# Performance work log

Measured on AMD Instinct MI355X. Metric: run time of the kernel, lower is better.

## Reference

```python
import jax, jax.numpy as jnp
import numpy as np

B, N, H, E, WF = 2048, 30, 256, 256, 32
TANH_C = 10.0  # tanh_exploration


def _mask_modify(m):
    # if a row is all True, un-mask the last column
    all_true = jnp.all(m, axis=1)
    return m.at[:, -1].set(m[:, -1] & ~all_true)


def _lstm_cell(x, h, c, W_ih, W_hh, b_ih, b_hh):
    gates = x @ W_ih.T + b_ih + h @ W_hh.T + b_hh
    i, f, g, o = jnp.split(gates, 4, axis=1)  # torch LSTMCell gate order
    c_new = jax.nn.sigmoid(f) * c + jax.nn.sigmoid(i) * jnp.tanh(g)
    h_new = jax.nn.sigmoid(o) * jnp.tanh(c_new)
    return h_new, c_new


def _attention(query, ref, Wq, bq, Wr, br, v, C=None):
    # query [B,H], ref [B,H,N] (context permuted)
    q = query @ Wq.T + bq                                        # [B,H]
    e = jnp.einsum('oh,bhn->bon', Wr, ref) + br[None, :, None]   # 1x1 conv
    u = jnp.einsum('h,bhn->bn', v, jnp.tanh(q[:, :, None] + e))  # [B,N]
    logits = C * jnp.tanh(u) if C is not None else u
    return e, logits


def setup_inputs() -> dict:
    key = jax.random.key(0)
    ks = jax.random.split(key, 24)
    s = 0.06  # ~1/sqrt(H) init scale
    n = lambda k, sh: jax.random.normal(k, sh, dtype=jnp.float32)
    return {
        'decoder_input': n(ks[0], (B, E)),
        'embedded_inputs': n(ks[1], (N, B, E)),
        'h0': n(ks[2], (B, H)),
        'c0': n(ks[3], (B, H)),
        'context': n(ks[4], (N, B, H)),
        'embed_cou': n(ks[5], (B, WF)),
        'D': jax.random.uniform(ks[6], (B, N, N), dtype=jnp.float32),
        'W_ih': n(ks[7], (4 * H, E)) * s,
        'W_hh': n(ks[8], (4 * H, H)) * s,
        'b_ih': n(ks[9], (4 * H,)) * s,
        'b_hh': n(ks[10], (4 * H,)) * s,
        'W_merge': n(ks[11], (H, H + WF)) * s,
        'b_merge': n(ks[12], (H,)) * s,
        'Wq_p': n(ks[13], (H, H)) * s,
        'bq_p': n(ks[14], (H,)) * s,
        'Wr_p': n(ks[15], (H, H)) * s,
        'br_p': n(ks[16], (H,)) * s,
        'v_p': n(ks[17], (H,)) * s,
        'Wq_g': n(ks[18], (H, H)) * s,
        'bq_g': n(ks[19], (H,)) * s,
        'Wr_g': n(ks[20], (H, H)) * s,
        'br_g': n(ks[21], (H,)) * s,
        'v_g': n(ks[22], (H,)) * s,
        'V_reach_mask_t': jnp.zeros((B, N), dtype=bool),
        'start_idx': jax.random.randint(ks[23], (B,), 0, N),
        'k_min_nodes': 3,
    }


def reference(decoder_input, embedded_inputs, h0, c0, context, embed_cou, D,
              W_ih, W_hh, b_ih, b_hh, W_merge, b_merge,
              Wq_p, bq_p, Wr_p, br_p, v_p,
              Wq_g, bq_g, Wr_g, br_g, v_g,
              V_reach_mask_t, start_idx, k_min_nodes):
    ref = jnp.transpose(context, (1, 2, 0))  # [B,H,N]
    arangeB = jnp.arange(B)
    arangeN = jnp.arange(N)

    def step(carry, _):
        h, c, mask, idxs, dec_in, knn_row = carry
        # --- update_knn_mask ('n-1'): builds the row used at the NEXT step ---
        Eb = D[arangeB, idxs]                                  # [B,N]
        weighted = Eb * (~mask).astype(Eb.dtype)
        valid = jnp.sum(~mask, axis=1) > k_min_nodes
        far = jnp.argmax(weighted, axis=1)
        next_row = (arangeN[None, :] == far[:, None]) & valid[:, None]
        # --- recurrence: update_mask + check_mask ---
        lm = mask.at[arangeB, idxs].set(True)
        lm = _mask_modify(_mask_modify(lm))
        full_mask = lm | knn_row
        # LSTM step + worker-feature merge
        hy, cy = _lstm_cell(dec_in, h, c, W_ih, W_hh, b_ih, b_hh)
        g_l = jnp.concatenate([hy, embed_cou], axis=1) @ W_merge.T + b_merge
        # one glimpse (n_glimpses=1)
        e_g, lg = _attention(g_l, ref, Wq_g, bq_g, Wr_g, br_g, v_g)
        lg = jnp.where(full_mask, -jnp.inf, lg)
        g_l = jnp.einsum('bhn,bn->bh', e_g, jax.nn.softmax(lg, axis=1))
        # pointer (use_tanh with C)
        _, lp = _attention(g_l, ref, Wq_p, bq_p, Wr_p, br_p, v_p, C=TANH_C)
        lp = jnp.where(full_mask, -jnp.inf, lp)
        log_p = jax.nn.log_softmax(lp, axis=1)
        new_idxs = jnp.argmax(log_p, axis=1)  # greedy decode
        new_dec = embedded_inputs[new_idxs, arangeB]  # [B,E]
        return (hy, cy, lm, new_idxs, new_dec, next_row), (log_p, new_idxs)

    init = (h0, c0, V_reach_mask_t, start_idx, decoder_input,
            jnp.zeros_like(V_reach_mask_t))
    (_, _, mask, _, _, _), (logps, sels) = jax.lax.scan(step, init, None, length=N)
    return jnp.swapaxes(logps, 0, 1), jnp.swapaxes(sels, 0, 1), mask
```

## Files before the change

kernel.cpp:

```cpp
#include <hip/hip_runtime.h>
#include <hip/hip_bf16.h>
#include <math.h>

#define B 2048
#define NN 30
#define H 256
#define EDIM 256
#define G4 1024

typedef __attribute__((ext_vector_type(8))) short short8;
typedef __attribute__((ext_vector_type(4))) float f32x4;

__device__ __forceinline__ float fsig(float x) {
    return __fdividef(1.f, 1.f + __expf(-x));
}
__device__ __forceinline__ float ftanh(float x) {
    return 1.f - __fdividef(2.f, __expf(2.f * x) + 1.f);
}

__global__ __launch_bounds__(256)
void gemm_big(const float* __restrict__ A,
              const float* __restrict__ W0, const float* __restrict__ W1,
              const float* __restrict__ W2,
              const float* __restrict__ b0, const float* __restrict__ b1,
              const float* __restrict__ b2,
              float* __restrict__ C0, float* __restrict__ C1,
              float* __restrict__ C2)
{
    __shared__ __align__(16) float As[16][128];
    __shared__ __align__(16) float Ws[16][128];
    int tid = threadIdx.x;
    int tx = tid & 15, ty = (tid >> 4) & 15;

    int lin = blockIdx.y * 6 + blockIdx.x;
    int v = (lin & 7) * 360 + (lin >> 3);
    int m0 = (v / 6) << 7;
    int nblk = v % 6;
    int part = nblk >> 1;
    int nin = (nblk & 1) << 7;
    const float* W    = part == 0 ? W0 : part == 1 ? W1 : W2;
    const float* bias = part == 0 ? b0 : part == 1 ? b1 : b2;
    float* C          = part == 0 ? C0 : part == 1 ? C1 : C2;

    int lr = tid >> 1;
    int lk8 = (tid & 1) << 3;
    const float* arow = A + (long)(m0 + lr) * 256 + lk8;
    const float* wrow = W + (long)(nin + lr) * 256 + lk8;
    float4 a0 = *(const float4*)(arow);
    float4 a1 = *(const float4*)(arow + 4);
    float4 w0 = *(const float4*)(wrow);
    float4 w1 = *(const float4*)(wrow + 4);
    float acc[8][8] = {};

    for (int k0 = 0; k0 < 256; k0 += 16) {
        As[lk8 + 0][lr] = a0.x; As[lk8 + 1][lr] = a0.y;
        As[lk8 + 2][lr] = a0.z; As[lk8 + 3][lr] = a0.w;
        As[lk8 + 4][lr] = a1.x; As[lk8 + 5][lr] = a1.y;
        As[lk8 + 6][lr] = a1.z; As[lk8 + 7][lr] = a1.w;
        Ws[lk8 + 0][lr] = w0.x; Ws[lk8 + 1][lr] = w0.y;
        Ws[lk8 + 2][lr] = w0.z; Ws[lk8 + 3][lr] = w0.w;
        Ws[lk8 + 4][lr] = w1.x; Ws[lk8 + 5][lr] = w1.y;
        Ws[lk8 + 6][lr] = w1.z; Ws[lk8 + 7][lr] = w1.w;
        __syncthreads();
        if (k0 + 16 < 256) {
            a0 = *(const float4*)(arow + k0 + 16);
            a1 = *(const float4*)(arow + k0 + 20);
            w0 = *(const float4*)(wrow + k0 + 16);
            w1 = *(const float4*)(wrow + k0 + 20);
        }
        #pragma unroll
        for (int k = 0; k < 16; ++k) {
            float4 af0 = *(const float4*)&As[k][ty << 2];
            float4 af1 = *(const float4*)&As[k][64 + (ty << 2)];
            float4 wf0 = *(const float4*)&Ws[k][tx << 2];
            float4 wf1 = *(const float4*)&Ws[k][64 + (tx << 2)];
            float av[8] = {af0.x, af0.y, af0.z, af0.w, af1.x, af1.y, af1.z, af1.w};
            float wv[8] = {wf0.x, wf0.y, wf0.z, wf0.w, wf1.x, wf1.y, wf1.z, wf1.w};
            #pragma unroll
            for (int i = 0; i < 8; ++i)
                #pragma unroll
                for (int j = 0; j < 8; ++j)
                    acc[i][j] = fmaf(av[i], wv[j], acc[i][j]);
        }
        __syncthreads();
    }

    float bj[8];
    #pragma unroll
    for (int j = 0; j < 8; ++j) {
        int cj = nin + ((j < 4) ? (tx << 2) + j : 64 + (tx << 2) + j - 4);
        bj[j] = bias[cj];
    }
    #pragma unroll
    for (int i = 0; i < 8; ++i) {
        int m = m0 + ((i < 4) ? (ty << 2) + i : 64 + (ty << 2) + i - 4);
        float* crow = C + (long)m * 256 + nin;
        float4 v0 = make_float4(acc[i][0] + bj[0], acc[i][1] + bj[1],
                                acc[i][2] + bj[2], acc[i][3] + bj[3]);
        float4 v1 = make_float4(acc[i][4] + bj[4], acc[i][5] + bj[5],
                                acc[i][6] + bj[6], acc[i][7] + bj[7]);
        *(float4*)&crow[(tx << 2)] = v0;
        *(float4*)&crow[64 + (tx << 2)] = v1;
    }
}

__global__ __launch_bounds__(256)
void gates_mfma(const unsigned short* __restrict__ dhi, const unsigned short* __restrict__ dlo,
                const unsigned short* __restrict__ hhi, const unsigned short* __restrict__ hlo,
                const unsigned short* __restrict__ Whi, const unsigned short* __restrict__ Wlo,
                const float* __restrict__ bsum, const float* __restrict__ cin,
                float* __restrict__ hout, float* __restrict__ cout,
                unsigned short* __restrict__ hohi, unsigned short* __restrict__ holo)
{
    __shared__ __align__(16) unsigned short Ah[128][40];
    __shared__ __align__(16) unsigned short Al[128][40];
    __shared__ __align__(16) unsigned short Bh[64][40];
    __shared__ __align__(16) unsigned short Bl[64][40];

    int tid = threadIdx.x;
    int w = tid >> 6, l = tid & 63;
    int lin = blockIdx.x;
    int v = (lin & 7) * 32 + (lin >> 3);
    int m0 = (v >> 4) << 7;
    int u0 = (v & 15) << 4;

    int arow = tid >> 1;
    int akb  = (tid & 1) << 4;
    int brw  = tid >> 2;
    int bkb  = (tid & 3) << 3;
    int wrow = ((brw >> 4) << 8) + u0 + (brw & 15);
    const unsigned short* wph = Whi + (long)wrow * 512 + bkb;
    const unsigned short* wpl = Wlo + (long)wrow * 512 + bkb;

    int fk = (l >> 4) << 3;
    int fr = l & 15;

    f32x4 acc[2][4];
    #pragma unroll
    for (int i = 0; i < 2; ++i)
        #pragma unroll
        for (int j = 0; j < 4; ++j)
            acc[i][j] = (f32x4){0.f, 0.f, 0.f, 0.f};

    for (int kt = 0; kt < 16; ++kt) {
        int k0 = kt << 5;
        const unsigned short* sah; const unsigned short* sal; int kk;
        if (k0 < 256) { sah = dhi; sal = dlo; kk = k0; }
        else          { sah = hhi; sal = hlo; kk = k0 - 256; }
        long abase = (long)(m0 + arow) * 256 + kk + akb;
        short8 a0 = *(const short8*)&sah[abase];
        short8 a1 = *(const short8*)&sah[abase + 8];
        short8 a2 = *(const short8*)&sal[abase];
        short8 a3 = *(const short8*)&sal[abase + 8];
        short8 b0 = *(const short8*)&wph[k0];
        short8 b1 = *(const short8*)&wpl[k0];
        __syncthreads();
        *(short8*)&Ah[arow][akb]     = a0;
        *(short8*)&Ah[arow][akb + 8] = a1;
        *(short8*)&Al[arow][akb]     = a2;
        *(short8*)&Al[arow][akb + 8] = a3;
        *(short8*)&Bh[brw][bkb] = b0;
        *(short8*)&Bl[brw][bkb] = b1;
        __syncthreads();

        short8 aH[2], aL[2], bH[4], bL[4];
        #pragma unroll
        for (int ms = 0; ms < 2; ++ms) {
            int r = (w << 5) + (ms << 4) + fr;
            aH[ms] = *(const short8*)&Ah[r][fk];
            aL[ms] = *(const short8*)&Al[r][fk];
        }
        #pragma unroll
        for (int s = 0; s < 4; ++s) {
            int r = (s << 4) + fr;
            bH[s] = *(const short8*)&Bh[r][fk];
            bL[s] = *(const short8*)&Bl[r][fk];
        }
        #pragma unroll
        for (int ms = 0; ms < 2; ++ms)
            #pragma unroll
            for (int s = 0; s < 4; ++s)
                acc[ms][s] = __builtin_amdgcn_mfma_f32_16x16x32_bf16(aH[ms], bH[s], acc[ms][s], 0, 0, 0);
        #pragma unroll
        for (int ms = 0; ms < 2; ++ms)
            #pragma unroll
            for (int s = 0; s < 4; ++s)
                acc[ms][s] = __builtin_amdgcn_mfma_f32_16x16x32_bf16(aH[ms], bL[s], acc[ms][s], 0, 0, 0);
        #pragma unroll
        for (int ms = 0; ms < 2; ++ms)
            #pragma unroll
            for (int s = 0; s < 4; ++s)
                acc[ms][s] = __builtin_amdgcn_mfma_f32_16x16x32_bf16(aL[ms], bH[s], acc[ms][s], 0, 0, 0);
    }

    int u = u0 + fr;
    float bI = bsum[u], bF = bsum[256 + u], bG = bsum[512 + u], bO = bsum[768 + u];
    #pragma unroll
    for (int ms = 0; ms < 2; ++ms) {
        #pragma unroll
        for (int r = 0; r < 4; ++r) {
            int m = m0 + (w << 5) + (ms << 4) + ((l >> 4) << 2) + r;
            float gi = acc[ms][0][r] + bI;
            float gf = acc[ms][1][r] + bF;
            float gg = acc[ms][2][r] + bG;
            float go = acc[ms][3][r] + bO;
            float cv = cin[(long)m * H + u];
            float cn = fsig(gf) * cv + fsig(gi) * ftanh(gg);
            float hn = fsig(go) * ftanh(cn);
            cout[(long)m * H + u] = cn;
            hout[(long)m * H + u] = hn;
            unsigned hb = __float_as_uint(hn);
            hohi[(long)m * H + u] = (unsigned short)(hb >> 16);
            float lo = hn - __uint_as_float(hb & 0xffff0000u);
            holo[(long)m * H + u] = (unsigned short)(__float_as_uint(lo) >> 16);
        }
    }
}

__global__ __launch_bounds__(256)
void gemm_qg(const float* __restrict__ A, const float* __restrict__ W,
             const float* __restrict__ addend, float* __restrict__ C)
{
    __shared__ __align__(16) float As[2][16][36];
    __shared__ __align__(16) float Ws[2][16][68];
    int tid = threadIdx.x;
    int tx = tid & 15, ty = tid >> 4;

    int lin = blockIdx.y * 4 + blockIdx.x;
    int v = (lin & 7) * 32 + (lin >> 3);
    int m0 = (v >> 2) << 5;
    int n0 = (v & 3) << 6;

    int lrA = tid >> 3, lkA = (tid & 7) << 1;
    int lrW = tid >> 2, lkW = (tid & 3) << 2;
    const float* arow = A + (long)(m0 + lrA) * 256;
    const float* wrow = W + (long)(n0 + lrW) * 256;

    float2 av = *(const float2*)(arow + lkA);
    float4 wv = *(const float4*)(wrow + lkW);
    As[0][lkA + 0][lrA] = av.x; As[0][lkA + 1][lrA] = av.y;
    Ws[0][lkW + 0][lrW] = wv.x; Ws[0][lkW + 1][lrW] = wv.y;
    Ws[0][lkW + 2][lrW] = wv.z; Ws[0][lkW + 3][lrW] = wv.w;
    __syncthreads();

    float acc[2][4] = {};
    int p = 0;
    for (int k0 = 0; k0 < 256; k0 += 16) {
        float2 nav; float4 nwv;
        bool more = (k0 + 16) < 256;
        if (more) {
            nav = *(const float2*)(arow + k0 + 16 + lkA);
            nwv = *(const float4*)(wrow + k0 + 16 + lkW);
        }
        #pragma unroll
        for (int k = 0; k < 16; ++k) {
            float2 a2 = *(const float2*)&As[p][k][ty << 1];
            float4 b4 = *(const float4*)&Ws[p][k][tx << 2];
            acc[0][0] = fmaf(a2.x, b4.x, acc[0][0]);
            acc[0][1] = fmaf(a2.x, b4.y, acc[0][1]);
            acc[0][2] = fmaf(a2.x, b4.z, acc[0][2]);
            acc[0][3] = fmaf(a2.x, b4.w, acc[0][3]);
            acc[1][0] = fmaf(a2.y, b4.x, acc[1][0]);
            acc[1][1] = fmaf(a2.y, b4.y, acc[1][1]);
            acc[1][2] = fmaf(a2.y, b4.z, acc[1][2]);
            acc[1][3] = fmaf(a2.y, b4.w, acc[1][3]);
        }
        if (more) {
            int q = p ^ 1;
            As[q][lkA + 0][lrA] = nav.x; As[q][lkA + 1][lrA] = nav.y;
            Ws[q][lkW + 0][lrW] = nwv.x; Ws[q][lkW + 1][lrW] = nwv.y;
            Ws[q][lkW + 2][lrW] = nwv.z; Ws[q][lkW + 3][lrW] = nwv.w;
        }
        __syncthreads();
        p ^= 1;
    }

    #pragma unroll
    for (int i = 0; i < 2; ++i) {
        int m = m0 + (ty << 1) + i;
        const float* ad = &addend[(long)m * 256 + n0 + (tx << 2)];
        float4 adv = *(const float4*)ad;
        float4 o = make_float4(acc[i][0] + adv.x, acc[i][1] + adv.y,
                               acc[i][2] + adv.z, acc[i][3] + adv.w);
        *(float4*)&C[(long)m * 256 + n0 + (tx << 2)] = o;
    }
}

__global__ void init_state(const unsigned char* __restrict__ vr, const int* __restrict__ start,
                           unsigned char* __restrict__ mask, unsigned char* __restrict__ knn,
                           int* __restrict__ idxs)
{
    int t = blockIdx.x * 256 + threadIdx.x;
    if (t < B * NN) { mask[t] = vr[t] ? 1 : 0; knn[t] = 0; }
    if (t < B) idxs[t] = start[t];
}

__global__ void prep_wsplit(const float* __restrict__ Wih, const float* __restrict__ Whh,
                            const float* __restrict__ bih, const float* __restrict__ bhh,
                            unsigned short* __restrict__ Whi, unsigned short* __restrict__ Wlo,
                            float* __restrict__ bsum)
{
    int n = blockIdx.x, k = threadIdx.x;
    float a = Wih[(long)n * H + k];
    unsigned ab = __float_as_uint(a);
    Whi[(long)n * 512 + k] = (unsigned short)(ab >> 16);
    float alo = a - __uint_as_float(ab & 0xffff0000u);
    Wlo[(long)n * 512 + k] = (unsigned short)(__float_as_uint(alo) >> 16);
    float b = Whh[(long)n * H + k];
    unsigned bb = __float_as_uint(b);
    Whi[(long)n * 512 + 256 + k] = (unsigned short)(bb >> 16);
    float blo = b - __uint_as_float(bb & 0xffff0000u);
    Wlo[(long)n * 512 + 256 + k] = (unsigned short)(__float_as_uint(blo) >> 16);
    if (k == 0) bsum[n] = bih[n] + bhh[n];
}

__global__ void conv_pair(const float* __restrict__ x,
                          unsigned short* __restrict__ xhi, unsigned short* __restrict__ xlo)
{
    int t = blockIdx.x * 256 + threadIdx.x;
    float a = x[t];
    unsigned ab = __float_as_uint(a);
    xhi[t] = (unsigned short)(ab >> 16);
    float lo = a - __uint_as_float(ab & 0xffff0000u);
    xlo[t] = (unsigned short)(__float_as_uint(lo) >> 16);
}

__global__ void prep_compose1(const float* __restrict__ Wqg, const float* __restrict__ Wm,
                              float* __restrict__ W1c)
{
    int h = blockIdx.x, k = threadIdx.x;
    float a = 0.f;
    for (int j = 0; j < H; ++j) a = fmaf(Wqg[(long)h * H + j], Wm[(long)j * 288 + k], a);
    W1c[(long)h * H + k] = a;
}

__global__ void prep_compose2(const float* __restrict__ Wqg, const float* __restrict__ Wm,
                              const float* __restrict__ bm, const float* __restrict__ bqg,
                              float* __restrict__ W2c, float* __restrict__ bc)
{
    int h = blockIdx.x, w = threadIdx.x;
    if (w < 32) {
        float a = 0.f;
        for (int j = 0; j < H; ++j) a = fmaf(Wqg[(long)h * H + j], Wm[(long)j * 288 + 256 + w], a);
        W2c[h * 32 + w] = a;
    } else if (w == 32) {
        float a = 0.f;
        for (int j = 0; j < H; ++j) a = fmaf(Wqg[(long)h * H + j], bm[j], a);
        bc[h] = a + bqg[h];
    }
}

__global__ __launch_bounds__(256)
void prep_qc(const float* __restrict__ cou, const float* __restrict__ W2c,
             const float* __restrict__ bc, float* __restrict__ qc)
{
    __shared__ float sWT[32 * 256];
    __shared__ float sb[256];
    int b = blockIdx.x, h = threadIdx.x;
    for (int i = h; i < 32 * 256; i += 256) {
        int hh = i >> 5, ww = i & 31;
        sWT[ww * 256 + hh] = W2c[i];
    }
    sb[h] = bc[h];
    __syncthreads();
    const float* cr = cou + (long)b * 32;
    float a = sb[h];
    for (int w = 0; w < 32; ++w) a = fmaf(cr[w], sWT[w * 256 + h], a);
    qc[(long)b * H + h] = a;
}

__global__ void prep_composeF(const float* __restrict__ Wqp, const float* __restrict__ Wrg,
                              const float* __restrict__ brg, float* __restrict__ WFc,
                              float* __restrict__ bFc)
{
    int f = blockIdx.x, k = threadIdx.x;
    float a = 0.f;
    for (int j = 0; j < H; ++j) a = fmaf(Wqp[(long)f * H + j], Wrg[(long)j * H + k], a);
    WFc[(long)f * H + k] = a;
    if (k == 0) {
        float s = 0.f;
        for (int j = 0; j < H; ++j) s = fmaf(Wqp[(long)f * H + j], brg[j], s);
        bFc[f] = s;
    }
}

__global__ __launch_bounds__(512)
void mega_attn2(const float* __restrict__ eg, const float* __restrict__ ep,
                const float* __restrict__ F, const float* __restrict__ qg,
                const float* __restrict__ vg, const float* __restrict__ vp,
                const float* __restrict__ bqp,
                const float* __restrict__ D, const int* __restrict__ kminp,
                unsigned char* __restrict__ mask, unsigned char* __restrict__ knn,
                const float* __restrict__ emb,
                float* __restrict__ out, int step,
                int* __restrict__ idxs,
                unsigned short* __restrict__ dechi, unsigned short* __restrict__ declo)
{
    int b = blockIdx.x, tid = threadIdx.x;
    int wv = tid >> 6, lane = tid & 63;
    __shared__ float sU[32], sP[32];
    __shared__ float sQp[H];
    __shared__ float sPar[2][H];
    __shared__ unsigned char sFull[32];
    __shared__ int sSel;

    float4 q4  = ((const float4*)(qg + (long)b * H))[lane];
    float4 vg4 = ((const float4*)vg)[lane];
    float4 vp4 = ((const float4*)vp)[lane];

    if (tid < 64) {
        bool in = lane < NN;
        int idx = idxs[b];
        int kmin = *kminp;
        unsigned char m = in ? mask[b * NN + lane] : (unsigned char)1;
        float dv = in ? D[((long)b * NN + idx) * NN + lane] : 0.f;
        unsigned long long unm = __ballot(in && !m);
        int cnt = __popcll(unm);
        bool valid = cnt > kmin;
        float bw = (in && !m) ? dv : (in ? 0.f : -1.f);
        int bi = in ? lane : 1000;
        #pragma unroll
        for (int off = 32; off; off >>= 1) {
            float ow = __shfl_down(bw, off, 64);
            int oi = __shfl_down(bi, off, 64);
            if (ow > bw || (ow == bw && oi < bi)) { bw = ow; bi = oi; }
        }
        int far = __shfl(bi, 0, 64);
        unsigned char mnew = (in && lane == idx) ? 1 : m;
        #pragma unroll
        for (int rep = 0; rep < 2; ++rep) {
            bool allm = (__ballot(in && !mnew) == 0ull);
            if (allm && lane == NN - 1) mnew = 0;
        }
        unsigned char kn = in ? knn[b * NN + lane] : 0;
        if (in) {
            sFull[lane] = (mnew | kn) ? 1 : 0;
            mask[b * NN + lane] = mnew;
            knn[b * NN + lane] = (lane == far && valid) ? 1 : 0;
        }
    }
    __syncthreads();

    for (int n = wv; n < NN; n += 8) {
        if (sFull[n]) continue;
        float4 e4 = ((const float4*)(eg + ((long)n * B + b) * H))[lane];
        float s = vg4.x * ftanh(q4.x + e4.x);
        s = fmaf(vg4.y, ftanh(q4.y + e4.y), s);
        s = fmaf(vg4.z, ftanh(q4.z + e4.z), s);
        s = fmaf(vg4.w, ftanh(q4.w + e4.w), s);
        #pragma unroll
        for (int off = 32; off; off >>= 1) s += __shfl_down(s, off, 64);
        if (lane == 0) sU[n] = s;
    }
    __syncthreads();

    if (tid < 64) {
        bool in = tid < NN;
        bool f = in ? (sFull[tid] != 0) : true;
        float u = (in && !f) ? sU[tid] : -INFINITY;
        float mx = u;
        #pragma unroll
        for (int off = 32; off; off >>= 1) mx = fmaxf(mx, __shfl_down(mx, off, 64));
        mx = __shfl(mx, 0, 64);
        float p = (in && !f) ? __expf(u - mx) : 0.f;
        float sum = p;
        #pragma unroll
        for (int off = 32; off; off >>= 1) sum += __shfl_down(sum, off, 64);
        sum = __shfl(sum, 0, 64);
        if (in) sP[tid] = p / sum;
    }
    __syncthreads();

    {
        int half = tid >> 8, hh = tid & 255;
        float a = 0.f;
        #pragma unroll
        for (int n = 0; n < 15; ++n) {
            int nn = half * 15 + n;
            float pn = sP[nn];
            if (pn != 0.f)
                a = fmaf(pn, F[((long)nn * B + b) * H + hh], a);
        }
        sPar[half][hh] = a;
    }
    __syncthreads();
    if (tid < 256) sQp[tid] = bqp[tid] + sPar[0][tid] + sPar[1][tid];
    __syncthreads();

    float4 qp4 = ((const float4*)sQp)[lane];
    for (int n = wv; n < NN; n += 8) {
        if (sFull[n]) continue;
        float4 e4 = ((const float4*)(ep + ((long)n * B + b) * H))[lane];
        float s = vp4.x * ftanh(qp4.x + e4.x);
        s = fmaf(vp4.y, ftanh(qp4.y + e4.y), s);
        s = fmaf(vp4.z, ftanh(qp4.z + e4.z), s);
        s = fmaf(vp4.w, ftanh(qp4.w + e4.w), s);
        #pragma unroll
        for (int off = 32; off; off >>= 1) s += __shfl_down(s, off, 64);
        if (lane == 0) sU[n] = 10.f * ftanh(s);
    }
    __syncthreads();

    if (tid < 64) {
        bool in = tid < NN;
        bool f = in ? (sFull[tid] != 0) : true;
        float l = (in && !f) ? sU[tid] : -INFINITY;
        float mx = l; int bi = in ? tid : 1000;
        #pragma unroll
        for (int off = 32; off; off >>= 1) {
            float om = __shfl_down(mx, off, 64);
            int oi = __shfl_down(bi, off, 64);
            if (om > mx || (om == mx && oi < bi)) { mx = om; bi = oi; }
        }
        mx = __shfl(mx, 0, 64);
        bi = __shfl(bi, 0, 64);
        float pe = (in && !f) ? __expf(l - mx) : 0.f;
        float sum = pe;
        #pragma unroll
        for (int off = 32; off; off >>= 1) sum += __shfl_down(sum, off, 64);
        sum = __shfl(sum, 0, 64);
        float lse = mx + __logf(sum);
        if (tid == 0) {
            idxs[b] = bi;
            out[(long)B * NN * NN + (long)b * NN + step] = (float)bi;
            sSel = bi;
        }
        if (in)
            out[(long)b * NN * NN + (long)step * NN + tid] =
                f ? -1e30f : (l - lse);
    }
    __syncthreads();

    if (tid < 256) {
        int sel = sSel;
        float d = emb[((long)sel * B + b) * EDIM + tid];
        unsigned db = __float_as_uint(d);
        dechi[(long)b * H + tid] = (unsigned short)(db >> 16);
        float lo = d - __uint_as_float(db & 0xffff0000u);
        declo[(long)b * H + tid] = (unsigned short)(__float_as_uint(lo) >> 16);
    }
}

__global__ void mask_out(const unsigned char* __restrict__ mask, float* __restrict__ out)
{
    int t = blockIdx.x * 256 + threadIdx.x;
    if (t < B * NN)
        out[(long)B * NN * NN + (long)B * NN + t] = mask[t] ? 1.f : 0.f;
}

extern "C" void kernel_launch(void* const* d_in, const int* in_sizes, int n_in,
                              void* d_out, int out_size, void* d_ws, size_t ws_size,
                              hipStream_t stream)
{
    const float* decoder_input = (const float*)d_in[0];
    const float* embedded     = (const float*)d_in[1];
    const float* h0           = (const float*)d_in[2];
    const float* c0           = (const float*)d_in[3];
    const float* context      = (const float*)d_in[4];
    const float* embed_cou    = (const float*)d_in[5];
    const float* D            = (const float*)d_in[6];
    const float* W_ih         = (const float*)d_in[7];
    const float* W_hh         = (const float*)d_in[8];
    const float* b_ih         = (const float*)d_in[9];
    const float* b_hh         = (const float*)d_in[10];
    const float* W_merge      = (const float*)d_in[11];
    const float* b_merge      = (const float*)d_in[12];
    const float* Wq_p         = (const float*)d_in[13];
    const float* bq_p         = (const float*)d_in[14];
    const float* Wr_p         = (const float*)d_in[15];
    const float* br_p         = (const float*)d_in[16];
    const float* v_p          = (const float*)d_in[17];
    const float* Wq_g         = (const float*)d_in[18];
    const float* bq_g         = (const float*)d_in[19];
    const float* Wr_g         = (const float*)d_in[20];
    const float* br_g         = (const float*)d_in[21];
    const float* v_g          = (const float*)d_in[22];
    const unsigned char* vreach = (const unsigned char*)d_in[23];
    const int* start_idx      = (const int*)d_in[24];
    const int* kminp          = (const int*)d_in[25];

    float* ws = (float*)d_ws;
    size_t o = 0;
    float* eg     = ws + o; o += (size_t)B * NN * H;
    float* ep     = ws + o; o += (size_t)B * NN * H;
    float* Fbuf   = ws + o; o += (size_t)B * NN * H;
    float* hb0    = ws + o; o += (size_t)B * H;
    float* hb1    = ws + o; o += (size_t)B * H;
    float* cb0    = ws + o; o += (size_t)B * H;
    float* cb1    = ws + o; o += (size_t)B * H;
    float* qbuf   = ws + o; o += (size_t)B * H;
    float* qc     = ws + o; o += (size_t)B * H;
    float* W1c    = ws + o; o += (size_t)H * H;
    float* W2c    = ws + o; o += (size_t)H * 32;
    float* bc     = ws + o; o += (size_t)H;
    float* WFc    = ws + o; o += (size_t)H * H;
    float* bFc    = ws + o; o += (size_t)H;
    float* bsum   = ws + o; o += (size_t)G4;
    unsigned short* Whi  = (unsigned short*)(ws + o); o += (size_t)G4 * 512 / 2;
    unsigned short* Wlo  = (unsigned short*)(ws + o); o += (size_t)G4 * 512 / 2;
    unsigned short* dechi = (unsigned short*)(ws + o); o += (size_t)B * H / 2;
    unsigned short* declo = (unsigned short*)(ws + o); o += (size_t)B * H / 2;
    unsigned short* hAhi = (unsigned short*)(ws + o); o += (size_t)B * H / 2;
    unsigned short* hAlo = (unsigned short*)(ws + o); o += (size_t)B * H / 2;
    unsigned short* hBhi = (unsigned short*)(ws + o); o += (size_t)B * H / 2;
    unsigned short* hBlo = (unsigned short*)(ws + o); o += (size_t)B * H / 2;
    unsigned char* maskb = (unsigned char*)(ws + o);
    unsigned char* knnb  = maskb + (size_t)B * NN;
    int* idxs = (int*)(knnb + (size_t)B * NN + 64);

    float* out = (float*)d_out;

    init_state<<<dim3((B * NN + 255) / 256), dim3(256), 0, stream>>>(
        vreach, start_idx, maskb, knnb, idxs);

    prep_wsplit<<<dim3(G4), dim3(256), 0, stream>>>(W_ih, W_hh, b_ih, b_hh,
                                                    Whi, Wlo, bsum);
    conv_pair<<<dim3(B * H / 256), dim3(256), 0, stream>>>(decoder_input, dechi, declo);
    conv_pair<<<dim3(B * H / 256), dim3(256), 0, stream>>>(h0, hAhi, hAlo);
    prep_compose1<<<dim3(H), dim3(256), 0, stream>>>(Wq_g, W_merge, W1c);
    prep_compose2<<<dim3(H), dim3(64), 0, stream>>>(Wq_g, W_merge, b_merge, bq_g,
                                                    W2c, bc);
    prep_qc<<<dim3(B), dim3(256), 0, stream>>>(embed_cou, W2c, bc, qc);
    prep_composeF<<<dim3(H), dim3(256), 0, stream>>>(Wq_p, Wr_g, br_g, WFc, bFc);

    gemm_big<<<dim3(6, (B * NN) / 128), dim3(256), 0, stream>>>(
        context, Wr_g, Wr_p, WFc, br_g, br_p, bFc, eg, ep, Fbuf);

    const float* cin = c0;
    unsigned short* hInHi = hAhi; unsigned short* hInLo = hAlo;
    unsigned short* hOutHi = hBhi; unsigned short* hOutLo = hBlo;

    for (int step = 0; step < NN; ++step) {
        int p = step & 1;
        float* hout = p ? hb1 : hb0;
        float* cout = p ? cb1 : cb0;

        gates_mfma<<<dim3(256), dim3(256), 0, stream>>>(
            dechi, declo, hInHi, hInLo, Whi, Wlo, bsum, cin,
            hout, cout, hOutHi, hOutLo);

        gemm_qg<<<dim3(4, B / 32), dim3(256), 0, stream>>>(
            hout, W1c, qc, qbuf);

        mega_attn2<<<dim3(B), dim3(512), 0, stream>>>(
            eg, ep, Fbuf, qbuf, v_g, v_p, bq_p, D, kminp,
            maskb, knnb, embedded, out, step, idxs, dechi, declo);

        cin = cout;
        unsigned short* th = hInHi; hInHi = hOutHi; hOutHi = th;
        unsigned short* tl = hInLo; hInLo = hOutLo; hOutLo = tl;
    }

    mask_out<<<dim3((B * NN + 255) / 256), dim3(256), 0, stream>>>(maskb, out);
}
```

Before: 2.518 ms.

## Rewrite big FP32 GEMM with split-bf16 MFMA (3-way split, 6 products)

```diff
diff --git a/kernel.cpp b/kernel.cpp
--- a/kernel.cpp
+++ b/kernel.cpp
@@ -16,6 +16,18 @@
 }
 __device__ __forceinline__ float ftanh(float x) {
     return 1.f - __fdividef(2.f, __expf(2.f * x) + 1.f);
+}
+
+__device__ __forceinline__ void split3(float a, unsigned short& h,
+                                       unsigned short& m_, unsigned short& l_)
+{
+    unsigned ab = __float_as_uint(a);
+    h = (unsigned short)(ab >> 16);
+    float r1 = a - __uint_as_float(ab & 0xffff0000u);
+    unsigned rb = __float_as_uint(r1);
+    m_ = (unsigned short)(rb >> 16);
+    float r2 = r1 - __uint_as_float(rb & 0xffff0000u);
+    l_ = (unsigned short)(__float_as_uint(r2) >> 16);
 }
 
 __global__ __launch_bounds__(256)
@@ -27,10 +39,15 @@
               float* __restrict__ C0, float* __restrict__ C1,
               float* __restrict__ C2)
 {
-    __shared__ __align__(16) float As[16][128];
-    __shared__ __align__(16) float Ws[16][128];
+    __shared__ __align__(16) unsigned short Ah[128][40];
+    __shared__ __align__(16) unsigned short Am[128][40];
+    __shared__ __align__(16) unsigned short Al[128][40];
+    __shared__ __align__(16) unsigned short Bh[128][40];
+    __shared__ __align__(16) unsigned short Bm[128][40];
+    __shared__ __align__(16) unsigned short Bl[128][40];
+
     int tid = threadIdx.x;
-    int tx = tid & 15, ty = (tid >> 4) & 15;
+    int w = tid >> 6, l = tid & 63;
 
     int lin = blockIdx.y * 6 + blockIdx.x;
     int v = (lin & 7) * 360 + (lin >> 3);
@@ -42,65 +59,111 @@
     const float* bias = part == 0 ? b0 : part == 1 ? b1 : b2;
     float* C          = part == 0 ? C0 : part == 1 ? C1 : C2;
 
-    int lr = tid >> 1;
-    int lk8 = (tid & 1) << 3;
-    const float* arow = A + (long)(m0 + lr) * 256 + lk8;
-    const float* wrow = W + (long)(nin + lr) * 256 + lk8;
-    float4 a0 = *(const float4*)(arow);
-    float4 a1 = *(const float4*)(arow + 4);
-    float4 w0 = *(const float4*)(wrow);
-    float4 w1 = *(const float4*)(wrow + 4);
-    float acc[8][8] = {};
-
-    for (int k0 = 0; k0 < 256; k0 += 16) {
-        As[lk8 + 0][lr] = a0.x; As[lk8 + 1][lr] = a0.y;
-        As[lk8 + 2][lr] = a0.z; As[lk8 + 3][lr] = a0.w;
-        As[lk8 + 4][lr] = a1.x; As[lk8 + 5][lr] = a1.y;
-        As[lk8 + 6][lr] = a1.z; As[lk8 + 7][lr] = a1.w;
-        Ws[lk8 + 0][lr] = w0.x; Ws[lk8 + 1][lr] = w0.y;
-        Ws[lk8 + 2][lr] = w0.z; Ws[lk8 + 3][lr] = w0.w;
-        Ws[lk8 + 4][lr] = w1.x; Ws[lk8 + 5][lr] = w1.y;
-        Ws[lk8 + 6][lr] = w1.z; Ws[lk8 + 7][lr] = w1.w;
+    int srow = tid >> 1;
+    int skb  = (tid & 1) << 4;
+    const float* arow = A + (long)(m0 + srow) * 256 + skb;
+    const float* wrow = W + (long)(nin + srow) * 256 + skb;
+
+    int fr = l & 15;
+    int fk = (l >> 4) << 3;
+
+    f32x4 acc[2][8];
+    #pragma unroll
+    for (int i = 0; i < 2; ++i)
+        #pragma unroll
+        for (int j = 0; j < 8; ++j)
+            acc[i][j] = (f32x4){0.f, 0.f, 0.f, 0.f};
+
+    for (int kt = 0; kt < 8; ++kt) {
+        int k0 = kt << 5;
+        float4 a4[4], w4[4];
+        #pragma unroll
+        for (int i = 0; i < 4; ++i) {
+            a4[i] = *(const float4*)(arow + k0 + (i << 2));
+            w4[i] = *(const float4*)(wrow + k0 + (i << 2));
+        }
         __syncthreads();
-        if (k0 + 16 < 256) {
-            a0 = *(const float4*)(arow + k0 + 16);
-            a1 = *(const float4*)(arow + k0 + 20);
-            w0 = *(const float4*)(wrow + k0 + 16);
-            w1 = *(const float4*)(wrow + k0 + 20);
-        }
-        #pragma unroll
-        for (int k = 0; k < 16; ++k) {
-            float4 af0 = *(const float4*)&As[k][ty << 2];
-            float4 af1 = *(const float4*)&As[k][64 + (ty << 2)];
-            float4 wf0 = *(const float4*)&Ws[k][tx << 2];
-            float4 wf1 = *(const float4*)&Ws[k][64 + (tx << 2)];
-            float av[8] = {af0.x, af0.y, af0.z, af0.w, af1.x, af1.y, af1.z, af1.w};
-            float wv[8] = {wf0.x, wf0.y, wf0.z, wf0.w, wf1.x, wf1.y, wf1.z, wf1.w};
-            #pragma unroll
-            for (int i = 0; i < 8; ++i)
+        #pragma unroll
+        for (int i = 0; i < 4; ++i) {
+            float va[4] = {a4[i].x, a4[i].y, a4[i].z, a4[i].w};
+            float vw[4] = {w4[i].x, w4[i].y, w4[i].z, w4[i].w};
+            #pragma unroll
+            for (int j = 0; j < 4; ++j) {
+                int c = skb + (i << 2) + j;
+                split3(va[j], Ah[srow][c], Am[srow][c], Al[srow][c]);
+                split3(vw[j], Bh[srow][c], Bm[srow][c], Bl[srow][c]);
+            }
+        }
+        __syncthreads();
+
+        short8 aH[2], aM[2], aL[2];
+        #pragma unroll
+        for (int ms = 0; ms < 2; ++ms) {
+            int r = (w << 5) + (ms << 4) + fr;
+            aH[ms] = *(const short8*)&Ah[r][fk];
+            aM[ms] = *(const short8*)&Am[r][fk];
+            aL[ms] = *(const short8*)&Al[r][fk];
+        }
+        #pragma unroll
+        for (int ng = 0; ng < 2; ++ng) {
+            short8 bH[4], bM[4], bL[4];
+            #pragma unroll
+            for (int j = 0; j < 4; ++j) {
+                int r = (((ng << 2) + j) << 4) + fr;
+                bH[j] = *(const short8*)&Bh[r][fk];
+                bM[j] = *(const short8*)&Bm[r][fk];
+                bL[j] = *(const short8*)&Bl[r][fk];
+            }
+            #pragma unroll
+            for (int ms = 0; ms < 2; ++ms)
                 #pragma unroll
-                for (int j = 0; j < 8; ++j)
-                    acc[i][j] = fmaf(av[i], wv[j], acc[i][j]);
-        }
-        __syncthreads();
-    }
-
-    float bj[8];
+                for (int j = 0; j < 4; ++j)
+                    acc[ms][(ng << 2) + j] = __builtin_amdgcn_mfma_f32_16x16x32_bf16(
+                        aH[ms], bH[j], acc[ms][(ng << 2) + j], 0, 0, 0);
+            #pragma unroll
+            for (int ms = 0; ms < 2; ++ms)
+                #pragma unroll
+                for (int j = 0; j < 4; ++j)
+                    acc[ms][(ng << 2) + j] = __builtin_amdgcn_mfma_f32_16x16x32_bf16(
+                        aH[ms], bM[j], acc[ms][(ng << 2) + j], 0, 0, 0);
+            #pragma unroll
+            for (int ms = 0; ms < 2; ++ms)
+                #pragma unroll
+                for (int j = 0; j < 4; ++j)
+                    acc[ms][(ng << 2) + j] = __builtin_amdgcn_mfma_f32_16x16x32_bf16(
+                        aM[ms], bH[j], acc[ms][(ng << 2) + j], 0, 0, 0);
+            #pragma unroll
+            for (int ms = 0; ms < 2; ++ms)
+                #pragma unroll
+                for (int j = 0; j < 4; ++j)
+                    acc[ms][(ng << 2) + j] = __builtin_amdgcn_mfma_f32_16x16x32_bf16(
+                        aH[ms], bL[j], acc[ms][(ng << 2) + j], 0, 0, 0);
+            #pragma unroll
+            for (int ms = 0; ms < 2; ++ms)
+                #pragma unroll
+                for (int j = 0; j < 4; ++j)
+                    acc[ms][(ng << 2) + j] = __builtin_amdgcn_mfma_f32_16x16x32_bf16(
+                        aM[ms], bM[j], acc[ms][(ng << 2) + j], 0, 0, 0);
+            #pragma unroll
+            for (int ms = 0; ms < 2; ++ms)
+                #pragma unroll
+                for (int j = 0; j < 4; ++j)
+                    acc[ms][(ng << 2) + j] = __builtin_amdgcn_mfma_f32_16x16x32_bf16(
+                        aL[ms], bH[j], acc[ms][(ng << 2) + j], 0, 0, 0);
+        }
+    }
+
     #pragma unroll
-    for (int j = 0; j < 8; ++j) {
-        int cj = nin + ((j < 4) ? (tx << 2) + j : 64 + (tx << 2) + j - 4);
-        bj[j] = bias[cj];
-    }
-    #pragma unroll
-    for (int i = 0; i < 8; ++i) {
-        int m = m0 + ((i < 4) ? (ty << 2) + i : 64 + (ty << 2) + i - 4);
-        float* crow = C + (long)m * 256 + nin;
-        float4 v0 = make_float4(acc[i][0] + bj[0], acc[i][1] + bj[1],
-                                acc[i][2] + bj[2], acc[i][3] + bj[3]);
-        float4 v1 = make_float4(acc[i][4] + bj[4], acc[i][5] + bj[5],
-                                acc[i][6] + bj[6], acc[i][7] + bj[7]);
-        *(float4*)&crow[(tx << 2)] = v0;
-        *(float4*)&crow[64 + (tx << 2)] = v1;
+    for (int ms = 0; ms < 2; ++ms) {
+        #pragma unroll
+        for (int ns = 0; ns < 8; ++ns) {
+            float bv = bias[nin + (ns << 4) + fr];
+            #pragma unroll
+            for (int r = 0; r < 4; ++r) {
+                int m = m0 + (w << 5) + (ms << 4) + ((l >> 4) << 2) + r;
+                C[(long)m * 256 + nin + (ns << 4) + fr] = acc[ms][ns][r] + bv;
+            }
+        }
     }
 }
 
```

After: 2.383 ms. -5.4%, faster.
